# Performance work log

Measured on AMD Instinct MI355X. Metric: run time of the kernel, lower is better.

## Reference

```python
import jax, jax.numpy as jnp
import numpy as np

NODE_NUM = 20000
NUM_CENTROIDS = 64
EMBED_SIZE = 128
EPS = 1e-5
POINT_SCALE = 0.1 / np.sqrt(EMBED_SIZE)  # keep Poincare-ball norms << 1


def setup_inputs() -> dict:
    key = jax.random.key(0)
    k1, k2 = jax.random.split(key)
    node_repr = jax.random.normal(k1, (NODE_NUM, EMBED_SIZE), dtype=jnp.float32) * POINT_SCALE
    centroid_weight = jax.random.normal(k2, (NUM_CENTROIDS, EMBED_SIZE), dtype=jnp.float32) * POINT_SCALE
    mask = jnp.ones((NODE_NUM, 1), dtype=jnp.float32)
    return {"node_repr": node_repr, "mask": mask, "centroid_weight": centroid_weight}


def _poincare_pairwise_dist(u, v):
    # u: [N, E], v: [C, E] -> [N, C]
    # d(u,v) = arccosh(1 + 2*||u-v||^2 / ((1-||u||^2)(1-||v||^2)))
    su = jnp.sum(u * u, axis=-1)                      # [N]
    sv = jnp.sum(v * v, axis=-1)                      # [C]
    dot = jnp.einsum('ne,ce->nc', u, v)               # [N, C]
    sqdist = su[:, None] + sv[None, :] - 2.0 * dot    # ||u-v||^2, [N, C]
    sqdist = jnp.maximum(sqdist, 0.0)
    denom = jnp.maximum((1.0 - su)[:, None] * (1.0 - sv)[None, :], EPS)
    arg = jnp.maximum(1.0 + 2.0 * sqdist / denom, 1.0 + EPS)
    return jnp.arccosh(arg)


def reference(node_repr, mask, centroid_weight):
    node_num = node_repr.shape[0]
    num_centroids = centroid_weight.shape[0]
    # fused pairwise manifold distance, no [N*C, E] materialization
    dist = _poincare_pairwise_dist(node_repr, centroid_weight)      # [N, C]
    node_centroid_dist = dist[None, :, :] * mask[None, :, :]        # [1, N, C] (mask broadcasts [N,1])
    graph_centroid_dist = jnp.sum(node_centroid_dist, axis=1) / jnp.sum(mask)  # [1, C]
    return (graph_centroid_dist, node_centroid_dist)
```

## Files before the change

### kernel.cpp

```cpp
#include <hip/hip_runtime.h>
#include <hip/hip_bf16.h>
#include <math.h>

#define EMBED  128
#define NUM_C  64
#define EPS    1e-5f
#define NPB    32
#define LDSROW 132

typedef __attribute__((ext_vector_type(8))) short bf16x8;
typedef __attribute__((ext_vector_type(4))) float f32x4;

__device__ __forceinline__ bf16x8 pack8(float4 x, float4 y) {
    __hip_bfloat162 p0 = __float22bfloat162_rn(float2{x.x, x.y});
    __hip_bfloat162 p1 = __float22bfloat162_rn(float2{x.z, x.w});
    __hip_bfloat162 p2 = __float22bfloat162_rn(float2{y.x, y.y});
    __hip_bfloat162 p3 = __float22bfloat162_rn(float2{y.z, y.w});
    union { __hip_bfloat162 h[4]; bf16x8 v; } u;
    u.h[0] = p0; u.h[1] = p1; u.h[2] = p2; u.h[3] = p3;
    return u.v;
}

__global__ __launch_bounds__(256) void cd_main(
    const float* __restrict__ node_repr,
    const float* __restrict__ mask,
    const float* __restrict__ cent,
    float* __restrict__ out,
    float* __restrict__ wcol,
    float* __restrict__ wmsk,
    int N, int nb, int atomicMode)
{
    __shared__ float sa[NPB * LDSROW];
    __shared__ float s_su[NPB];
    __shared__ float s_ms[NPB];

    const int tid  = threadIdx.x;
    const int lane = tid & 63;
    const int wv   = tid >> 6;
    const int quad = lane >> 4;
    const int lm   = lane & 15;
    const int cw   = wv * 16;
    const int node0 = blockIdx.x * NPB;

    const int srow = tid >> 3;
    const int scol = (tid & 7) * 16;
    {
        int row = node0 + srow;
        int rc  = row < N ? row : N - 1;
        const float* p = node_repr + (long)rc * EMBED + scol;
        float4 r0 = *(const float4*)(p);
        float4 r1 = *(const float4*)(p + 4);
        float4 r2 = *(const float4*)(p + 8);
        float4 r3 = *(const float4*)(p + 12);
        float mrow = (row < N) ? mask[rc] : 0.f;

        float* dst = &sa[srow * LDSROW + scol];
        *(float4*)(dst)      = r0;
        *(float4*)(dst + 4)  = r1;
        *(float4*)(dst + 8)  = r2;
        *(float4*)(dst + 12) = r3;

        float pp = 0.f;
        pp = fmaf(r0.x,r0.x, fmaf(r0.y,r0.y, fmaf(r0.z,r0.z, fmaf(r0.w,r0.w, pp))));
        pp = fmaf(r1.x,r1.x, fmaf(r1.y,r1.y, fmaf(r1.z,r1.z, fmaf(r1.w,r1.w, pp))));
        pp = fmaf(r2.x,r2.x, fmaf(r2.y,r2.y, fmaf(r2.z,r2.z, fmaf(r2.w,r2.w, pp))));
        pp = fmaf(r3.x,r3.x, fmaf(r3.y,r3.y, fmaf(r3.z,r3.z, fmaf(r3.w,r3.w, pp))));
        pp += __shfl_xor(pp, 1); pp += __shfl_xor(pp, 2); pp += __shfl_xor(pp, 4);
        if ((tid & 7) == 0) { s_su[srow] = pp; s_ms[srow] = mrow; }
    }

    const float* bp = cent + (long)(cw + lm) * EMBED + quad * 8;
    float svp = 0.f;
    bf16x8 bb[4];
    #pragma unroll
    for (int ks = 0; ks < 4; ++ks) {
        float4 b0 = *(const float4*)(bp + ks * 32);
        float4 b1 = *(const float4*)(bp + ks * 32 + 4);
        svp = fmaf(b0.x,b0.x, fmaf(b0.y,b0.y, fmaf(b0.z,b0.z, fmaf(b0.w,b0.w, svp))));
        svp = fmaf(b1.x,b1.x, fmaf(b1.y,b1.y, fmaf(b1.z,b1.z, fmaf(b1.w,b1.w, svp))));
        bb[ks] = pack8(b0, b1);
    }
    svp += __shfl_xor(svp, 16); svp += __shfl_xor(svp, 32);
    const float sv1 = 1.f - svp;

    __syncthreads();

    f32x4 acc0 = {0.f,0.f,0.f,0.f}, acc1 = {0.f,0.f,0.f,0.f};
    #pragma unroll
    for (int ks = 0; ks < 4; ++ks) {
        const int base = quad * 8 + ks * 32;
        float4 a00 = *(const float4*)&sa[lm * LDSROW + base];
        float4 a01 = *(const float4*)&sa[lm * LDSROW + base + 4];
        float4 a10 = *(const float4*)&sa[(16 + lm) * LDSROW + base];
        float4 a11 = *(const float4*)&sa[(16 + lm) * LDSROW + base + 4];
        acc0 = __builtin_amdgcn_mfma_f32_16x16x32_bf16(pack8(a00, a01), bb[ks], acc0, 0, 0, 0);
        acc1 = __builtin_amdgcn_mfma_f32_16x16x32_bf16(pack8(a10, a11), bb[ks], acc1, 0, 0, 0);
    }

    float gcol = 0.f;
    #pragma unroll
    for (int r = 0; r < 4; ++r) {
        const int m0 = quad * 4 + r;
        {
            const int n = node0 + m0;
            const float su_m = s_su[m0];
            const float mk_m = s_ms[m0];
            float sq    = fmaxf(su_m + svp - 2.f * acc0[r], 0.f);
            float denom = fmaxf((1.f - su_m) * sv1, EPS);
            float tt    = fmaxf(2.f * sq / denom, EPS);
            float v     = __logf(1.f + tt + sqrtf(tt * (tt + 2.f))) * mk_m;
            if (n < N) { out[NUM_C + (long)n * NUM_C + cw + lm] = v; gcol += v; }
        }
        {
            const int n = node0 + 16 + m0;
            const float su_m = s_su[16 + m0];
            const float mk_m = s_ms[16 + m0];
            float sq    = fmaxf(su_m + svp - 2.f * acc1[r], 0.f);
            float denom = fmaxf((1.f - su_m) * sv1, EPS);
            float tt    = fmaxf(2.f * sq / denom, EPS);
            float v     = __logf(1.f + tt + sqrtf(tt * (tt + 2.f))) * mk_m;
            if (n < N) { out[NUM_C + (long)n * NUM_C + cw + lm] = v; gcol += v; }
        }
    }

    gcol += __shfl_xor(gcol, 16); gcol += __shfl_xor(gcol, 32);
    if (quad == 0) {
        if (atomicMode) atomicAdd(&wcol[cw + lm], gcol);
        else            wcol[(long)(cw + lm) * nb + blockIdx.x] = gcol;
    }
    if (wv == 0) {
        float ms = (lane < NPB) ? s_ms[lane] : 0.f;
        #pragma unroll
        for (int k = 32; k; k >>= 1) ms += __shfl_xor(ms, k, 64);
        if (lane == 0) {
            if (atomicMode) atomicAdd(&wmsk[0], ms);
            else            wmsk[blockIdx.x] = ms;
        }
    }
}

__global__ __launch_bounds__(256) void cd_fin1(
    const float* __restrict__ wcol, const float* __restrict__ wmsk,
    float* __restrict__ out, int nb)
{
    __shared__ float rs[4], rm[4];
    const int c   = blockIdx.x;
    const int tid = threadIdx.x;

    float s = 0.f, m = 0.f;
    for (int b = tid; b < nb; b += 256) {
        s += wcol[(long)c * nb + b];
        m += wmsk[b];
    }
    #pragma unroll
    for (int k = 32; k; k >>= 1) { s += __shfl_xor(s, k, 64); m += __shfl_xor(m, k, 64); }
    if ((tid & 63) == 0) { rs[tid >> 6] = s; rm[tid >> 6] = m; }
    __syncthreads();
    if (tid == 0)
        out[c] = (rs[0] + rs[1] + rs[2] + rs[3]) / (rm[0] + rm[1] + rm[2] + rm[3]);
}

__global__ void cd_zero(float* acc) { if (threadIdx.x < NUM_C + 1) acc[threadIdx.x] = 0.f; }
__global__ void cd_fin_atomic(const float* __restrict__ acc, float* __restrict__ out) {
    int c = threadIdx.x;
    if (c < NUM_C) out[c] = acc[c] / acc[NUM_C];
}

extern "C" void kernel_launch(void* const* d_in, const int* in_sizes, int n_in,
                              void* d_out, int out_size, void* d_ws, size_t ws_size,
                              hipStream_t stream) {
    const float* node_repr = (const float*)d_in[0];
    const float* mask      = (const float*)d_in[1];
    const float* cent      = (const float*)d_in[2];
    float* out = (float*)d_out;

    const int N  = in_sizes[0] / EMBED;
    const int nb = (N + NPB - 1) / NPB;
    const size_t needed = ((size_t)NUM_C * nb + nb) * sizeof(float);

    if (ws_size >= needed) {
        float* wcol = (float*)d_ws;
        float* wmsk = wcol + (size_t)NUM_C * nb;
        cd_main<<<nb, 256, 0, stream>>>(node_repr, mask, cent, out, wcol, wmsk, N, nb, 0);
        cd_fin1<<<NUM_C, 256, 0, stream>>>(wcol, wmsk, out, nb);
    } else {
        float* acc = (float*)d_ws;
        cd_zero<<<1, 128, 0, stream>>>(acc);
        cd_main<<<nb, 256, 0, stream>>>(node_repr, mask, cent, out, acc, acc + NUM_C, N, nb, 1);
        cd_fin_atomic<<<1, 64, 0, stream>>>(acc, out);
    }
}
```

Before: 72.50 us.

## Fuse final reduction into main kernel via banked atomics and last-block finish

Replaces the per-block partial-sum buffer and separate finalize kernel with atomic adds into 16 spread-out accumulator banks, plus a completion counter so the last block computes the graph-level means. A memset clears the banks and counter before launch. This removes one kernel launch and the strided partial-sum pass, at the cost of atomic contention and a threadfence/counter handshake. It also swaps the division for a hardware reciprocal, which is slightly less precise.

Result: slower. 90.92 us (+25.4%).

```diff
diff --git a/kernel.cpp b/kernel.cpp
--- a/kernel.cpp
+++ b/kernel.cpp
@@ -7,6 +7,8 @@
 #define EPS    1e-5f
 #define NPB    32
 #define LDSROW 132
+#define BANKS  16
+#define BSTRIDE 80
 
 typedef __attribute__((ext_vector_type(8))) short bf16x8;
 typedef __attribute__((ext_vector_type(4))) float f32x4;
@@ -26,13 +28,14 @@
     const float* __restrict__ mask,
     const float* __restrict__ cent,
     float* __restrict__ out,
-    float* __restrict__ wcol,
-    float* __restrict__ wmsk,
-    int N, int nb, int atomicMode)
+    float* __restrict__ acc,
+    unsigned* __restrict__ cnt,
+    int N, int nb)
 {
     __shared__ float sa[NPB * LDSROW];
     __shared__ float s_su[NPB];
     __shared__ float s_ms[NPB];
+    __shared__ unsigned s_last;
 
     const int tid  = threadIdx.x;
     const int lane = tid & 63;
@@ -107,7 +110,7 @@
             const float mk_m = s_ms[m0];
             float sq    = fmaxf(su_m + svp - 2.f * acc0[r], 0.f);
             float denom = fmaxf((1.f - su_m) * sv1, EPS);
-            float tt    = fmaxf(2.f * sq / denom, EPS);
+            float tt    = fmaxf(2.f * sq * __builtin_amdgcn_rcpf(denom), EPS);
             float v     = __logf(1.f + tt + sqrtf(tt * (tt + 2.f))) * mk_m;
             if (n < N) { out[NUM_C + (long)n * NUM_C + cw + lm] = v; gcol += v; }
         }
@@ -117,53 +120,41 @@
             const float mk_m = s_ms[16 + m0];
             float sq    = fmaxf(su_m + svp - 2.f * acc1[r], 0.f);
             float denom = fmaxf((1.f - su_m) * sv1, EPS);
-            float tt    = fmaxf(2.f * sq / denom, EPS);
+            float tt    = fmaxf(2.f * sq * __builtin_amdgcn_rcpf(denom), EPS);
             float v     = __logf(1.f + tt + sqrtf(tt * (tt + 2.f))) * mk_m;
             if (n < N) { out[NUM_C + (long)n * NUM_C + cw + lm] = v; gcol += v; }
         }
     }
 
     gcol += __shfl_xor(gcol, 16); gcol += __shfl_xor(gcol, 32);
-    if (quad == 0) {
-        if (atomicMode) atomicAdd(&wcol[cw + lm], gcol);
-        else            wcol[(long)(cw + lm) * nb + blockIdx.x] = gcol;
-    }
+    float* bank = acc + (blockIdx.x & (BANKS - 1)) * BSTRIDE;
+    if (quad == 0) atomicAdd(&bank[cw + lm], gcol);
     if (wv == 0) {
         float ms = (lane < NPB) ? s_ms[lane] : 0.f;
         #pragma unroll
         for (int k = 32; k; k >>= 1) ms += __shfl_xor(ms, k, 64);
-        if (lane == 0) {
-            if (atomicMode) atomicAdd(&wmsk[0], ms);
-            else            wmsk[blockIdx.x] = ms;
+        if (lane == 0) atomicAdd(&bank[64], ms);
+    }
+
+    __syncthreads();
+    if (tid == 0) {
+        __threadfence();
+        unsigned old = atomicAdd(cnt, 1u);
+        s_last = (old == (unsigned)(nb - 1)) ? 1u : 0u;
+    }
+    __syncthreads();
+    if (s_last) {
+        __threadfence();
+        if (tid < NUM_C) {
+            float s = 0.f, m = 0.f;
+            #pragma unroll
+            for (int b = 0; b < BANKS; ++b) {
+                s += acc[b * BSTRIDE + tid];
+                m += acc[b * BSTRIDE + 64];
+            }
+            out[tid] = s / m;
         }
     }
-}
-
-__global__ __launch_bounds__(256) void cd_fin1(
-    const float* __restrict__ wcol, const float* __restrict__ wmsk,
-    float* __restrict__ out, int nb)
-{
-    __shared__ float rs[4], rm[4];
-    const int c   = blockIdx.x;
-    const int tid = threadIdx.x;
-
-    float s = 0.f, m = 0.f;
-    for (int b = tid; b < nb; b += 256) {
-        s += wcol[(long)c * nb + b];
-        m += wmsk[b];
-    }
-    #pragma unroll
-    for (int k = 32; k; k >>= 1) { s += __shfl_xor(s, k, 64); m += __shfl_xor(m, k, 64); }
-    if ((tid & 63) == 0) { rs[tid >> 6] = s; rm[tid >> 6] = m; }
-    __syncthreads();
-    if (tid == 0)
-        out[c] = (rs[0] + rs[1] + rs[2] + rs[3]) / (rm[0] + rm[1] + rm[2] + rm[3]);
-}
-
-__global__ void cd_zero(float* acc) { if (threadIdx.x < NUM_C + 1) acc[threadIdx.x] = 0.f; }
-__global__ void cd_fin_atomic(const float* __restrict__ acc, float* __restrict__ out) {
-    int c = threadIdx.x;
-    if (c < NUM_C) out[c] = acc[c] / acc[NUM_C];
 }
 
 extern "C" void kernel_launch(void* const* d_in, const int* in_sizes, int n_in,
@@ -176,17 +167,10 @@
 
     const int N  = in_sizes[0] / EMBED;
     const int nb = (N + NPB - 1) / NPB;
-    const size_t needed = ((size_t)NUM_C * nb + nb) * sizeof(float);
 
-    if (ws_size >= needed) {
-        float* wcol = (float*)d_ws;
-        float* wmsk = wcol + (size_t)NUM_C * nb;
-        cd_main<<<nb, 256, 0, stream>>>(node_repr, mask, cent, out, wcol, wmsk, N, nb, 0);
-        cd_fin1<<<NUM_C, 256, 0, stream>>>(wcol, wmsk, out, nb);
-    } else {
-        float* acc = (float*)d_ws;
-        cd_zero<<<1, 128, 0, stream>>>(acc);
-        cd_main<<<nb, 256, 0, stream>>>(node_repr, mask, cent, out, acc, acc + NUM_C, N, nb, 1);
-        cd_fin_atomic<<<1, 64, 0, stream>>>(acc, out);
-    }
+    float*    acc = (float*)d_ws;
+    unsigned* cnt = (unsigned*)(acc + BANKS * BSTRIDE);
+
+    hipMemsetAsync(d_ws, 0, (BANKS * BSTRIDE + 1) * sizeof(float), stream);
+    cd_main<<<nb, 256, 0, stream>>>(node_repr, mask, cent, out, acc, cnt, N, nb);
 }
```
